# Kernel tuning notes

Measured on AMD Instinct MI355X. Metric: run time of the kernel, lower is better.

## Reference

```python
import jax, jax.numpy as jnp
import numpy as np
from jax import lax

K = 20
SLOPE = 0.01


def setup_inputs() -> dict:
    key = jax.random.key(0)
    k1, k2 = jax.random.split(key)
    x = jax.random.normal(k1, (8, 64, 4096), dtype=jnp.float32)
    # Conv2d(2*64, 64, kernel_size=1, bias=False) weight, squeezed to (out, in)
    W = jax.random.normal(k2, (64, 128), dtype=jnp.float32) * 0.05
    return {"x": x, "W": W}


def reference(x, W):
    # x: (B, C, N), W: (O, 2C)
    B, C, N = x.shape
    # --- knn: pairwise_distance[b,i,j] = -||x_i||^2 + 2 x_i.x_j - ||x_j||^2 ---
    xx = jnp.sum(x * x, axis=1)                      # (B, N)
    inner = jnp.einsum('bcn,bcm->bnm', x, x)         # (B, N, N)
    pdist = 2.0 * inner - xx[:, :, None] - xx[:, None, :]
    idx = lax.top_k(pdist, K)[1]                     # (B, N, K) neighbor indices
    # --- get_graph_feature: gather neighbors, diff + center concat ---
    x_t = jnp.transpose(x, (0, 2, 1))                # (B, N, C)
    neigh = x_t[jnp.arange(B)[:, None, None], idx]   # (B, N, K, C)
    center = x_t[:, :, None, :]                      # (B, N, 1, C)
    feat = jnp.concatenate(
        [neigh - center, jnp.broadcast_to(center, (B, N, K, C))], axis=-1
    )                                                # (B, N, K, 2C)
    # --- 1x1 conv (no bias) + LeakyReLU ---
    h = jnp.einsum('bnkd,od->bonk', feat, W)         # (B, O, N, K)
    h = jnp.where(h >= 0, h, SLOPE * h)
    # --- max over neighbors ---
    return jnp.max(h, axis=-1)                       # (B, O, N)
```

## Files before the change

kernel.cpp:

```cpp
#include <hip/hip_runtime.h>
#include <cfloat>

#define B_ 8
#define C_ 64
#define N_ 4096
#define K_ 20
#define MARGIN 0.08f
#define CAP 64

typedef float f32x4v  __attribute__((ext_vector_type(4)));
typedef float f32x16v __attribute__((ext_vector_type(16)));
typedef _Float16 f16x8 __attribute__((ext_vector_type(8)));
typedef unsigned long long u64;

#define OFF_IDX 131072
#define OFF_QG  2752512
#define OFF_P0  19529728
#define OFF_P1  23724032

__device__ __forceinline__ void gll16(const void* g, void* l) {
    __builtin_amdgcn_global_load_lds(
        (const __attribute__((address_space(1))) unsigned int*)g,
        (__attribute__((address_space(3))) unsigned int*)l, 16, 0, 0);
}

__global__ __launch_bounds__(256) void k_split(const float* __restrict__ x,
                                               unsigned short* __restrict__ p0,
                                               unsigned short* __restrict__ p1,
                                               float* __restrict__ xxn) {
    __shared__ double sred[256];
    int b = blockIdx.x & 7, mt = blockIdx.x >> 3;
    int tid = threadIdx.x;
    int seg = tid >> 5, ml = tid & 31;
    int m = mt * 32 + ml;
    const float* xb = x + (size_t)b * C_ * N_;
    double ss = 0.0;
    unsigned short h0[8], h1[8];
#pragma unroll
    for (int j = 0; j < 8; ++j) {
        float v = xb[(size_t)(seg * 8 + j) * N_ + m];
        ss += (double)v * (double)v;
        _Float16 a = (_Float16)v;
        float r = v - (float)a;
        _Float16 bq = (_Float16)(r * 4096.f);
        h0[j] = __builtin_bit_cast(unsigned short, a);
        h1[j] = __builtin_bit_cast(unsigned short, bq);
    }
    uint4 q0, q1;
    q0.x = h0[0] | (h0[1] << 16); q0.y = h0[2] | (h0[3] << 16);
    q0.z = h0[4] | (h0[5] << 16); q0.w = h0[6] | (h0[7] << 16);
    q1.x = h1[0] | (h1[1] << 16); q1.y = h1[2] | (h1[3] << 16);
    q1.z = h1[4] | (h1[5] << 16); q1.w = h1[6] | (h1[7] << 16);
    size_t o16 = (size_t)(b * 8 + seg) * N_ + m;
    ((uint4*)p0)[o16] = q0;
    ((uint4*)p1)[o16] = q1;
    sred[tid] = ss;
    __syncthreads();
    if (tid < 32) {
        double t = 0.0;
#pragma unroll
        for (int s = 0; s < 8; ++s) t += sred[s * 32 + tid];
        xxn[b * N_ + mt * 32 + tid] = (float)(-0.5 * t);
    }
}

__device__ __forceinline__ void score4(const char* sm, const float* xxs,
                                       int mlb, int mf, int h,
                                       const f16x8 b0[4], float s[16]) {
    f32x16v acc;
#pragma unroll
    for (int g2i = 0; g2i < 4; ++g2i) {
        f32x4v xv = *(const f32x4v*)&xxs[mlb + 4 * h + 8 * g2i];
#pragma unroll
        for (int q = 0; q < 4; ++q) acc[g2i * 4 + q] = xv[q];
    }
    __builtin_amdgcn_s_setprio(1);
#pragma unroll
    for (int kc = 0; kc < 4; ++kc) {
        int seg = kc * 2 + h;
        f16x8 a0 = __builtin_bit_cast(f16x8,
            *(const f32x4v*)(sm + seg * 4096 + (mlb + mf) * 16));
        acc = __builtin_amdgcn_mfma_f32_32x32x16_f16(a0, b0[kc], acc, 0, 0, 0);
    }
    __builtin_amdgcn_s_setprio(0);
#pragma unroll
    for (int r = 0; r < 16; ++r) s[r] = acc[r];
}

__device__ __forceinline__ void score16(const char* sm, const float* xxs,
                                        int mlb, int mf, int h,
                                        const f16x8 b0[4], const f16x8 b1[4],
                                        float s[16]) {
    const float c12 = 1.f / 4096.f;
    f32x16v acc1, acc2;
#pragma unroll
    for (int g2i = 0; g2i < 4; ++g2i) {
        f32x4v xv = *(const f32x4v*)&xxs[mlb + 4 * h + 8 * g2i];
#pragma unroll
        for (int q = 0; q < 4; ++q) {
            acc1[g2i * 4 + q] = xv[q];
            acc2[g2i * 4 + q] = 0.f;
        }
    }
    __builtin_amdgcn_s_setprio(1);
#pragma unroll
    for (int kc = 0; kc < 4; ++kc) {
        int seg = kc * 2 + h;
        const char* pA = sm + seg * 4096 + (mlb + mf) * 16;
        f16x8 a0 = __builtin_bit_cast(f16x8, *(const f32x4v*)pA);
        f16x8 a1 = __builtin_bit_cast(f16x8, *(const f32x4v*)(pA + 32768));
        acc1 = __builtin_amdgcn_mfma_f32_32x32x16_f16(a0, b0[kc], acc1, 0, 0, 0);
        acc2 = __builtin_amdgcn_mfma_f32_32x32x16_f16(a0, b1[kc], acc2, 0, 0, 0);
        acc2 = __builtin_amdgcn_mfma_f32_32x32x16_f16(a1, b0[kc], acc2, 0, 0, 0);
    }
    __builtin_amdgcn_s_setprio(0);
#pragma unroll
    for (int r = 0; r < 16; ++r)
        s[r] = acc1[r] + acc2[r] * c12;
}

__global__ __launch_bounds__(512, 4) void k_topk(const unsigned short* __restrict__ p0g,
                                                 const unsigned short* __restrict__ p1g,
                                                 const float* __restrict__ xxn,
                                                 u64* bufg,
                                                 int* __restrict__ idxo,
                                                 const float* __restrict__ x,
                                                 const float* __restrict__ W,
                                                 float* qg) {
    __shared__ __align__(16) char smem[67328];
    int b = blockIdx.x & 7, nt = blockIdx.x >> 3;
    int n0 = nt * 64;
    int tid = threadIdx.x;
    int w = tid >> 6, l = tid & 63, h = l >> 5, mf = l & 31;
    int cs = w >> 1, wg = w & 1;
    int rowl = wg * 32 + mf;
    int b8 = b * 8;
    const f32x4v* g0 = (const f32x4v*)p0g;
    const f32x4v* g1 = (const f32x4v*)p1g;
    float* Mp   = (float*)(smem + 32768);
    float* xxs  = (float*)(smem + 65792);
    int*   cntp = (int*)(smem + 66816);
    float* T2p  = (float*)(smem + 67072);

    f16x8 b0[4], b1[4];
#pragma unroll
    for (int kc = 0; kc < 4; ++kc) {
        int seg = kc * 2 + h;
        size_t gi = (size_t)(b8 + seg) * N_ + n0 + rowl;
        b0[kc] = __builtin_bit_cast(f16x8, g0[gi]);
        b1[kc] = __builtin_bit_cast(f16x8, g1[gi]);
    }

#pragma unroll 1
    for (int ch = 0; ch < 16; ++ch) {
        __syncthreads();
#pragma unroll
        for (int i = 0; i < 4; ++i) {
            int lin = i * 512 + tid;
            int seg = lin >> 8, ml = lin & 255;
            gll16(g0 + ((size_t)(b8 + seg) * N_ + ch * 256 + ml),
                  smem + seg * 4096 + ml * 16);
        }
        if (tid < 256) xxs[tid] = xxn[b * N_ + ch * 256 + tid];
        __syncthreads();
#pragma unroll
        for (int t = 0; t < 2; ++t) {
            int mlb = cs * 64 + t * 32;
            float s[16];
            score4(smem, xxs, mlb, mf, h, b0, s);
            float m8[8];
#pragma unroll
            for (int r = 0; r < 8; ++r) m8[r] = fmaxf(s[r], s[r + 8]);
            float mx = fmaxf(fmaxf(fmaxf(m8[0], m8[1]), fmaxf(m8[2], m8[3])),
                             fmaxf(fmaxf(m8[4], m8[5]), fmaxf(m8[6], m8[7])));
            mx = fmaxf(mx, __shfl_xor(mx, 32));
            if (l < 32)
                Mp[rowl * 129 + ch * 8 + t * 4 + cs] = mx;
        }
    }

    __syncthreads();
    if (tid < 256) {
        int row = tid >> 2, q = tid & 3;
        const float* mrow = Mp + row * 129 + q * 32;
        float v8[8];
#pragma unroll
        for (int j = 0; j < 8; ++j) v8[j] = -FLT_MAX;
#pragma unroll
        for (int i = 0; i < 32; ++i) {
            float v = mrow[i];
#pragma unroll
            for (int j = 7; j >= 1; --j) {
                bool c1 = v > v8[j - 1];
                float nv = c1 ? v8[j - 1] : v;
                v8[j] = (v > v8[j]) ? nv : v8[j];
            }
            v8[0] = fmaxf(v8[0], v);
        }
        float* lp = (float*)smem + row * 33 + q * 8;
#pragma unroll
        for (int j = 0; j < 8; ++j) lp[j] = v8[j];
    }
    __syncthreads();
    if (tid < 64) {
        const float* lp = (const float*)smem + tid * 33;
        float hv0 = lp[0], hv1 = lp[8], hv2 = lp[16], hv3 = lp[24];
        int p0 = 0, p1 = 0, p2 = 0, p3 = 0;
        float tstar = -FLT_MAX;
        for (int k = 0; k < 20; ++k) {
            bool a = hv0 >= hv1; float ma = a ? hv0 : hv1; int sa = a ? 0 : 1;
            bool bb = hv2 >= hv3; float mb = bb ? hv2 : hv3; int sb = bb ? 2 : 3;
            bool c = ma >= mb; tstar = c ? ma : mb; int sl = c ? sa : sb;
            if (sl == 0) { ++p0; hv0 = (p0 < 8) ? lp[p0] : -FLT_MAX; }
            else if (sl == 1) { ++p1; hv1 = (p1 < 8) ? lp[8 + p1] : -FLT_MAX; }
            else if (sl == 2) { ++p2; hv2 = (p2 < 8) ? lp[16 + p2] : -FLT_MAX; }
            else { ++p3; hv3 = (p3 < 8) ? lp[24 + p3] : -FLT_MAX; }
        }
        T2p[tid] = tstar - MARGIN;
        cntp[tid] = 0;
    }
    __syncthreads();
    float T2r = T2p[rowl];

#pragma unroll 1
    for (int ch = 0; ch < 16; ++ch) {
        __syncthreads();
#pragma unroll
        for (int i = 0; i < 8; ++i) {
            int lin = i * 512 + tid;
            int panel = lin >> 11;
            int rem = lin & 2047;
            int seg = rem >> 8, ml = rem & 255;
            const f32x4v* src = panel ? g1 : g0;
            gll16(src + ((size_t)(b8 + seg) * N_ + ch * 256 + ml),
                  smem + panel * 32768 + seg * 4096 + ml * 16);
        }
        if (tid < 256) xxs[tid] = xxn[b * N_ + ch * 256 + tid];
        __syncthreads();
#pragma unroll
        for (int t = 0; t < 2; ++t) {
            int mlb = cs * 64 + t * 32;
            float s[16];
            score16(smem, xxs, mlb, mf, h, b0, b1, s);
            unsigned msk = 0;
#pragma unroll
            for (int r = 0; r < 16; ++r) msk |= (s[r] >= T2r) ? (1u << r) : 0u;
            int cb = ch * 256 + mlb + 4 * h;
            while (msk) {
                int r = __ffs(msk) - 1;
                msk &= msk - 1;
                int cand = cb + (r & 3) + 8 * (r >> 2);
                float sv = s[r];
                unsigned sb = __float_as_uint(sv);
                unsigned kk = (sv < 0.f) ? ~sb : (sb | 0x80000000u);
                int slot = atomicAdd(cntp + rowl, 1);
                if (slot < CAP)
                    bufg[((size_t)(b * N_ + n0 + rowl)) * CAP + slot] =
                        ((u64)kk << 32) | (unsigned)(~cand);
            }
        }
    }

    __syncthreads();
    u64*   keys = (u64*)(smem + 33536);
    float* Wl   = (float*)smem;
#pragma unroll
    for (int i = 0; i < 8; ++i) {
        int p = i * 512 + tid;
        int row = p >> 6, slot = p & 63;
        int c_ = cntp[row]; c_ = (c_ > CAP) ? CAP : c_;
        u64 key = 0;
        if (slot < c_)
            key = bufg[((size_t)(b * N_ + n0 + row)) * CAP + slot];
        keys[row * (CAP + 1) + slot] = key;
    }
#pragma unroll
    for (int i = 0; i < 16; ++i) {
        int lin = i * 512 + tid;
        int c = lin & 63, o2 = lin >> 6;
        float wv;
        if (o2 < 64) wv = W[o2 * 128 + c];
        else { int o = o2 - 64; wv = W[o * 128 + 64 + c] - W[o * 128 + c]; }
        Wl[c * 129 + o2] = wv;
    }
    __syncthreads();

    if (tid < 64) {
        int c_ = cntp[tid]; c_ = (c_ > CAP) ? CAP : c_;
        u64* kp = keys + tid * (CAP + 1);
        int* op = idxo + ((size_t)b * N_ + n0 + tid) * K_;
        for (int k = 0; k < K_; ++k) {
            u64 best = 0; int bs = 0;
            for (int s2 = 0; s2 < c_; ++s2) {
                bool g = kp[s2] > best;
                best = g ? kp[s2] : best;
                bs = g ? s2 : bs;
            }
            op[k] = (int)(~(unsigned)best) & 0xFFF;
            kp[bs] = 0;
        }
    }

    {
        int u = l, g8 = w;
        const float* xb = x + (size_t)b * C_ * N_ + n0 + g8 * 8;
        float a0[8], a1[8];
#pragma unroll
        for (int j = 0; j < 8; ++j) { a0[j] = 0.f; a1[j] = 0.f; }
#pragma unroll 4
        for (int c = 0; c < 64; ++c) {
            float2 wv = *(const float2*)&Wl[c * 129 + 2 * u];
            float4 v0 = *(const float4*)&xb[(size_t)c * N_];
            float4 v1 = *(const float4*)&xb[(size_t)c * N_ + 4];
            a0[0] += wv.x * v0.x; a1[0] += wv.y * v0.x;
            a0[1] += wv.x * v0.y; a1[1] += wv.y * v0.y;
            a0[2] += wv.x * v0.z; a1[2] += wv.y * v0.z;
            a0[3] += wv.x * v0.w; a1[3] += wv.y * v0.w;
            a0[4] += wv.x * v1.x; a1[4] += wv.y * v1.x;
            a0[5] += wv.x * v1.y; a1[5] += wv.y * v1.y;
            a0[6] += wv.x * v1.z; a1[6] += wv.y * v1.z;
            a0[7] += wv.x * v1.w; a1[7] += wv.y * v1.w;
        }
#pragma unroll
        for (int j = 0; j < 8; ++j) {
            float2 o; o.x = a0[j]; o.y = a1[j];
            *(float2*)&qg[((size_t)b * N_ + n0 + g8 * 8 + j) * 128 + 2 * u] = o;
        }
    }
}

__global__ __launch_bounds__(256) void k_out(const float* __restrict__ qg,
                                             const int* __restrict__ idxi,
                                             float* __restrict__ out) {
    __shared__ float T[16][66];
    int b = blockIdx.x & 7, nt = blockIdx.x >> 3;
    int n0 = nt * 16;
    int tid = threadIdx.x;
    int w = tid >> 6, o = tid & 63;
    const float* qgb = qg + (size_t)b * N_ * 128;
    for (int i = 0; i < 4; ++i) {
        int nl = w * 4 + i;
        int n = n0 + nl;
        const int* ip = idxi + ((size_t)b * N_ + n) * K_;
        int iks[K_];
#pragma unroll
        for (int k = 0; k < K_; ++k) iks[k] = ip[k];
        float gv = qgb[(size_t)n * 128 + 64 + o];
        float hh[K_];
#pragma unroll
        for (int k = 0; k < K_; ++k)
            hh[k] = qgb[(size_t)iks[k] * 128 + o];
#pragma unroll
        for (int k = 0; k < K_; ++k) {
            float v = hh[k] + gv;
            hh[k] = (v >= 0.f) ? v : 0.01f * v;
        }
        float m0 = fmaxf(fmaxf(fmaxf(hh[0], hh[1]), fmaxf(hh[2], hh[3])),
                         fmaxf(hh[4], hh[5]));
        float m1 = fmaxf(fmaxf(fmaxf(hh[6], hh[7]), fmaxf(hh[8], hh[9])),
                         fmaxf(hh[10], hh[11]));
        float m2 = fmaxf(fmaxf(fmaxf(hh[12], hh[13]), fmaxf(hh[14], hh[15])),
                         fmaxf(hh[16], hh[17]));
        float m3 = fmaxf(hh[18], hh[19]);
        T[nl][o] = fmaxf(fmaxf(m0, m1), fmaxf(m2, m3));
    }
    __syncthreads();
    int ow = tid >> 2, q = tid & 3;
    {
        int nl = q * 4;
        float4 v;
        v.x = T[nl + 0][ow]; v.y = T[nl + 1][ow];
        v.z = T[nl + 2][ow]; v.w = T[nl + 3][ow];
        *(float4*)&out[((size_t)b * 64 + ow) * N_ + n0 + nl] = v;
    }
}

extern "C" void kernel_launch(void* const* d_in, const int* in_sizes, int n_in,
                              void* d_out, int out_size, void* d_ws, size_t ws_size,
                              hipStream_t stream) {
    const float* x = (const float*)d_in[0];
    const float* W = (const float*)d_in[1];
    float* out = (float*)d_out;

    float*          xxn  = (float*)d_ws;
    int*            idx  = (int*)((char*)d_ws + OFF_IDX);
    float*          qg   = (float*)((char*)d_ws + OFF_QG);
    u64*            bufg = (u64*)((char*)d_ws + OFF_QG);
    unsigned short* p0   = (unsigned short*)((char*)d_ws + OFF_P0);
    unsigned short* p1   = (unsigned short*)((char*)d_ws + OFF_P1);

    k_split<<<dim3(1024), dim3(256), 0, stream>>>(x, p0, p1, xxn);
    k_topk <<<dim3(512), dim3(512), 0, stream>>>(p0, p1, xxn, bufg, idx, x, W, qg);
    k_out  <<<dim3(2048), dim3(256), 0, stream>>>(qg, idx, out);
}
```

Before: 207.0 us.

## Fuse split, top-k and output kernels into one persistent kernel with grid barriers

Merges the three kernel launches into a single 512-block kernel that does the fp16 split, the top-k/projection stage and the gather-max output stage in sequence, separated by a software grid barrier built on an atomic counter. The aim is to remove launch gaps and inter-kernel drain and fill between short stages. In exchange it relies on all 512 blocks being co-resident, since the spin barrier deadlocks otherwise. The split and output stages also run on fewer, larger blocks than before, which may lower their parallelism.

```diff
diff --git a/kernel.cpp b/kernel.cpp
--- a/kernel.cpp
+++ b/kernel.cpp
@@ -7,6 +7,7 @@
 #define K_ 20
 #define MARGIN 0.08f
 #define CAP 64
+#define GRID_ 512
 
 typedef float f32x4v  __attribute__((ext_vector_type(4)));
 typedef float f32x16v __attribute__((ext_vector_type(16)));
@@ -18,50 +19,27 @@
 #define OFF_P0  19529728
 #define OFF_P1  23724032
 
+__device__ unsigned g_ctr;
+
 __device__ __forceinline__ void gll16(const void* g, void* l) {
     __builtin_amdgcn_global_load_lds(
         (const __attribute__((address_space(1))) unsigned int*)g,
         (__attribute__((address_space(3))) unsigned int*)l, 16, 0, 0);
 }
 
-__global__ __launch_bounds__(256) void k_split(const float* __restrict__ x,
-                                               unsigned short* __restrict__ p0,
-                                               unsigned short* __restrict__ p1,
-                                               float* __restrict__ xxn) {
-    __shared__ double sred[256];
-    int b = blockIdx.x & 7, mt = blockIdx.x >> 3;
-    int tid = threadIdx.x;
-    int seg = tid >> 5, ml = tid & 31;
-    int m = mt * 32 + ml;
-    const float* xb = x + (size_t)b * C_ * N_;
-    double ss = 0.0;
-    unsigned short h0[8], h1[8];
-#pragma unroll
-    for (int j = 0; j < 8; ++j) {
-        float v = xb[(size_t)(seg * 8 + j) * N_ + m];
-        ss += (double)v * (double)v;
-        _Float16 a = (_Float16)v;
-        float r = v - (float)a;
-        _Float16 bq = (_Float16)(r * 4096.f);
-        h0[j] = __builtin_bit_cast(unsigned short, a);
-        h1[j] = __builtin_bit_cast(unsigned short, bq);
-    }
-    uint4 q0, q1;
-    q0.x = h0[0] | (h0[1] << 16); q0.y = h0[2] | (h0[3] << 16);
-    q0.z = h0[4] | (h0[5] << 16); q0.w = h0[6] | (h0[7] << 16);
-    q1.x = h1[0] | (h1[1] << 16); q1.y = h1[2] | (h1[3] << 16);
-    q1.z = h1[4] | (h1[5] << 16); q1.w = h1[6] | (h1[7] << 16);
-    size_t o16 = (size_t)(b * 8 + seg) * N_ + m;
-    ((uint4*)p0)[o16] = q0;
-    ((uint4*)p1)[o16] = q1;
-    sred[tid] = ss;
-    __syncthreads();
-    if (tid < 32) {
-        double t = 0.0;
-#pragma unroll
-        for (int s = 0; s < 8; ++s) t += sred[s * 32 + tid];
-        xxn[b * N_ + mt * 32 + tid] = (float)(-0.5 * t);
-    }
+__device__ __forceinline__ void gbarrier() {
+    __syncthreads();
+    if (threadIdx.x == 0) {
+        __threadfence();
+        unsigned t = __hip_atomic_fetch_add(&g_ctr, 1u, __ATOMIC_ACQ_REL,
+                                            __HIP_MEMORY_SCOPE_AGENT);
+        unsigned target = (t & ~(unsigned)(GRID_ - 1)) + GRID_;
+        while (__hip_atomic_load(&g_ctr, __ATOMIC_RELAXED,
+                                 __HIP_MEMORY_SCOPE_AGENT) < target)
+            __builtin_amdgcn_s_sleep(8);
+        __threadfence();
+    }
+    __syncthreads();
 }
 
 __device__ __forceinline__ void score4(const char* sm, const float* xxs,
@@ -119,14 +97,15 @@
         s[r] = acc1[r] + acc2[r] * c12;
 }
 
-__global__ __launch_bounds__(512, 4) void k_topk(const unsigned short* __restrict__ p0g,
-                                                 const unsigned short* __restrict__ p1g,
-                                                 const float* __restrict__ xxn,
-                                                 u64* bufg,
-                                                 int* __restrict__ idxo,
-                                                 const float* __restrict__ x,
-                                                 const float* __restrict__ W,
-                                                 float* qg) {
+__global__ __launch_bounds__(512, 4) void k_fused(const float* __restrict__ x,
+                                                  const float* __restrict__ W,
+                                                  unsigned short* p0g,
+                                                  unsigned short* p1g,
+                                                  float* xxn,
+                                                  u64* bufg,
+                                                  int* idxo,
+                                                  float* qg,
+                                                  float* __restrict__ out) {
     __shared__ __align__(16) char smem[67328];
     int b = blockIdx.x & 7, nt = blockIdx.x >> 3;
     int n0 = nt * 64;
@@ -135,12 +114,48 @@
     int cs = w >> 1, wg = w & 1;
     int rowl = wg * 32 + mf;
     int b8 = b * 8;
-    const f32x4v* g0 = (const f32x4v*)p0g;
-    const f32x4v* g1 = (const f32x4v*)p1g;
+    f32x4v* g0 = (f32x4v*)p0g;
+    f32x4v* g1 = (f32x4v*)p1g;
     float* Mp   = (float*)(smem + 32768);
     float* xxs  = (float*)(smem + 65792);
     int*   cntp = (int*)(smem + 66816);
     float* T2p  = (float*)(smem + 67072);
+
+    {
+        int seg = tid >> 6, mcol = tid & 63;
+        int m = n0 + mcol;
+        const float* xb = x + (size_t)b * C_ * N_;
+        double ss = 0.0;
+        unsigned short h0[8], h1[8];
+#pragma unroll
+        for (int j = 0; j < 8; ++j) {
+            float v = xb[(size_t)(seg * 8 + j) * N_ + m];
+            ss += (double)v * (double)v;
+            _Float16 a = (_Float16)v;
+            float r = v - (float)a;
+            _Float16 bq = (_Float16)(r * 4096.f);
+            h0[j] = __builtin_bit_cast(unsigned short, a);
+            h1[j] = __builtin_bit_cast(unsigned short, bq);
+        }
+        uint4 q0, q1;
+        q0.x = h0[0] | (h0[1] << 16); q0.y = h0[2] | (h0[3] << 16);
+        q0.z = h0[4] | (h0[5] << 16); q0.w = h0[6] | (h0[7] << 16);
+        q1.x = h1[0] | (h1[1] << 16); q1.y = h1[2] | (h1[3] << 16);
+        q1.z = h1[4] | (h1[5] << 16); q1.w = h1[6] | (h1[7] << 16);
+        size_t o16 = (size_t)(b8 + seg) * N_ + m;
+        ((uint4*)p0g)[o16] = q0;
+        ((uint4*)p1g)[o16] = q1;
+        double* sred = (double*)smem;
+        sred[tid] = ss;
+        __syncthreads();
+        if (tid < 64) {
+            double t = 0.0;
+#pragma unroll
+            for (int s = 0; s < 8; ++s) t += sred[s * 64 + tid];
+            xxn[b * N_ + n0 + tid] = (float)(-0.5 * t);
+        }
+    }
+    gbarrier();
 
     f16x8 b0[4], b1[4];
 #pragma unroll
@@ -327,51 +342,49 @@
             *(float2*)&qg[((size_t)b * N_ + n0 + g8 * 8 + j) * 128 + 2 * u] = o;
         }
     }
-}
-
-__global__ __launch_bounds__(256) void k_out(const float* __restrict__ qg,
-                                             const int* __restrict__ idxi,
-                                             float* __restrict__ out) {
-    __shared__ float T[16][66];
-    int b = blockIdx.x & 7, nt = blockIdx.x >> 3;
-    int n0 = nt * 16;
-    int tid = threadIdx.x;
-    int w = tid >> 6, o = tid & 63;
-    const float* qgb = qg + (size_t)b * N_ * 128;
-    for (int i = 0; i < 4; ++i) {
-        int nl = w * 4 + i;
-        int n = n0 + nl;
-        const int* ip = idxi + ((size_t)b * N_ + n) * K_;
-        int iks[K_];
-#pragma unroll
-        for (int k = 0; k < K_; ++k) iks[k] = ip[k];
-        float gv = qgb[(size_t)n * 128 + 64 + o];
-        float hh[K_];
-#pragma unroll
-        for (int k = 0; k < K_; ++k)
-            hh[k] = qgb[(size_t)iks[k] * 128 + o];
-#pragma unroll
-        for (int k = 0; k < K_; ++k) {
-            float v = hh[k] + gv;
-            hh[k] = (v >= 0.f) ? v : 0.01f * v;
-        }
-        float m0 = fmaxf(fmaxf(fmaxf(hh[0], hh[1]), fmaxf(hh[2], hh[3])),
-                         fmaxf(hh[4], hh[5]));
-        float m1 = fmaxf(fmaxf(fmaxf(hh[6], hh[7]), fmaxf(hh[8], hh[9])),
-                         fmaxf(hh[10], hh[11]));
-        float m2 = fmaxf(fmaxf(fmaxf(hh[12], hh[13]), fmaxf(hh[14], hh[15])),
-                         fmaxf(hh[16], hh[17]));
-        float m3 = fmaxf(hh[18], hh[19]);
-        T[nl][o] = fmaxf(fmaxf(m0, m1), fmaxf(m2, m3));
-    }
-    __syncthreads();
-    int ow = tid >> 2, q = tid & 3;
+    gbarrier();
+
     {
-        int nl = q * 4;
-        float4 v;
-        v.x = T[nl + 0][ow]; v.y = T[nl + 1][ow];
-        v.z = T[nl + 2][ow]; v.w = T[nl + 3][ow];
-        *(float4*)&out[((size_t)b * 64 + ow) * N_ + n0 + nl] = v;
+        float* T = (float*)smem;
+        int ww = tid >> 6, o = tid & 63;
+        const float* qgb = qg + (size_t)b * N_ * 128;
+#pragma unroll 1
+        for (int i = 0; i < 8; ++i) {
+            int nl = ww * 8 + i;
+            int n = n0 + nl;
+            const int* ip = idxo + ((size_t)b * N_ + n) * K_;
+            int iks[K_];
+#pragma unroll
+            for (int k = 0; k < K_; ++k) iks[k] = ip[k];
+            float gv = qgb[(size_t)n * 128 + 64 + o];
+            float hh[K_];
+#pragma unroll
+            for (int k = 0; k < K_; ++k)
+                hh[k] = qgb[(size_t)iks[k] * 128 + o];
+#pragma unroll
+            for (int k = 0; k < K_; ++k) {
+                float v = hh[k] + gv;
+                hh[k] = (v >= 0.f) ? v : 0.01f * v;
+            }
+            float m0 = fmaxf(fmaxf(fmaxf(hh[0], hh[1]), fmaxf(hh[2], hh[3])),
+                             fmaxf(hh[4], hh[5]));
+            float m1 = fmaxf(fmaxf(fmaxf(hh[6], hh[7]), fmaxf(hh[8], hh[9])),
+                             fmaxf(hh[10], hh[11]));
+            float m2 = fmaxf(fmaxf(fmaxf(hh[12], hh[13]), fmaxf(hh[14], hh[15])),
+                             fmaxf(hh[16], hh[17]));
+            float m3 = fmaxf(hh[18], hh[19]);
+            T[nl * 66 + o] = fmaxf(fmaxf(m0, m1), fmaxf(m2, m3));
+        }
+        __syncthreads();
+        int ow = tid >> 3, q = tid & 7;
+        int nl = q * 8;
+        float4 v0, v1;
+        v0.x = T[(nl + 0) * 66 + ow]; v0.y = T[(nl + 1) * 66 + ow];
+        v0.z = T[(nl + 2) * 66 + ow]; v0.w = T[(nl + 3) * 66 + ow];
+        v1.x = T[(nl + 4) * 66 + ow]; v1.y = T[(nl + 5) * 66 + ow];
+        v1.z = T[(nl + 6) * 66 + ow]; v1.w = T[(nl + 7) * 66 + ow];
+        *(float4*)&out[((size_t)b * 64 + ow) * N_ + n0 + nl] = v0;
+        *(float4*)&out[((size_t)b * 64 + ow) * N_ + n0 + nl + 4] = v1;
     }
 }
 
@@ -389,7 +402,6 @@
     unsigned short* p0   = (unsigned short*)((char*)d_ws + OFF_P0);
     unsigned short* p1   = (unsigned short*)((char*)d_ws + OFF_P1);
 
-    k_split<<<dim3(1024), dim3(256), 0, stream>>>(x, p0, p1, xxn);
-    k_topk <<<dim3(512), dim3(512), 0, stream>>>(p0, p1, xxn, bufg, idx, x, W, qg);
-    k_out  <<<dim3(2048), dim3(256), 0, stream>>>(qg, idx, out);
-}
+    k_fused<<<dim3(GRID_), dim3(512), 0, stream>>>(
+        x, W, p0, p1, xxn, bufg, idx, qg, out);
+}
```

Result: slower. 304.2 us (+46.9%).
